# Performance work log

Hardware: AMD Instinct MI355X
Metric: run time of the kernel (lower is better)

## Reference

```python
import jax, jax.numpy as jnp
import numpy as np

N = 50000
E = 800000
IN_DIM, HID, LAT, DEC_HID = 256, 256, 128, 512


def _glorot(key, shape):
    fan_in, fan_out = shape
    lim = np.sqrt(6.0 / (fan_in + fan_out))
    return jax.random.uniform(key, shape, jnp.float32, -lim, lim)


def setup_inputs() -> dict:
    key = jax.random.key(0)
    ks = jax.random.split(key, 10)
    x = jax.random.normal(ks[0], (N, IN_DIM), jnp.float32)
    edge_index = jax.random.randint(ks[1], (2, E), 0, N, dtype=jnp.int64)
    return {
        "x": x,
        "edge_index": edge_index,
        "W1": _glorot(ks[2], (IN_DIM, HID)), "b1": jnp.zeros((HID,), jnp.float32),
        "W2": _glorot(ks[3], (HID, LAT)), "b2": jnp.zeros((LAT,), jnp.float32),
        "Wd1": _glorot(ks[4], (LAT, DEC_HID)), "bd1": jnp.zeros((DEC_HID,), jnp.float32),
        "Wd2": _glorot(ks[5], (DEC_HID, IN_DIM)), "bd2": jnp.zeros((IN_DIM,), jnp.float32),
    }


def _gcn_layer(x, src, dst, W, b, num_nodes):
    # linear transform
    xt = x @ W + b                      # [N, out]
    # scatter-mean aggregation over incoming edges (PyG aggr='mean')
    msg = xt[src]                       # [E, out] gather of source features
    summed = jax.ops.segment_sum(msg, dst, num_segments=num_nodes)
    cnt = jax.ops.segment_sum(jnp.ones((src.shape[0],), xt.dtype), dst,
                              num_segments=num_nodes)
    mean = summed / jnp.maximum(cnt, 1.0)[:, None]   # 0 for isolated nodes
    # relu + residual
    return jax.nn.relu(mean) + xt


def reference(x, edge_index, W1, b1, W2, b2, Wd1, bd1, Wd2, bd2):
    src, dst = edge_index[0], edge_index[1]
    h = _gcn_layer(x, src, dst, W1, b1, x.shape[0])
    z = _gcn_layer(h, src, dst, W2, b2, x.shape[0])
    # decoder MLP
    x_hat = jax.nn.relu(z @ Wd1 + bd1) @ Wd2 + bd2
    return (x_hat, z)
```

## Files before the change

### kernel.cpp

```cpp
#include <hip/hip_runtime.h>
#include <hip/hip_bf16.h>

#define TPB 256

typedef __attribute__((ext_vector_type(8))) short short8;
typedef __attribute__((ext_vector_type(4))) float f32x4;

__device__ __forceinline__ unsigned short f2bf(float f) {
    unsigned int u = __float_as_uint(f);
    u = (u + 0x7FFFu + ((u >> 16) & 1u)) >> 16;
    return (unsigned short)u;
}
__device__ __forceinline__ float bflo(unsigned int u) { return __uint_as_float(u << 16); }
__device__ __forceinline__ float bfhi(unsigned int u) { return __uint_as_float(u & 0xFFFF0000u); }

__device__ __forceinline__ void gload16(const void* g, void* l) {
    __builtin_amdgcn_global_load_lds(
        (const __attribute__((address_space(1))) unsigned int*)g,
        (__attribute__((address_space(3))) unsigned int*)l, 16, 0, 0);
}

__global__ void transpose_convert_all(
    const float* __restrict__ Wa, unsigned short* __restrict__ Ta, int Ka, int Na,
    const float* __restrict__ Wb, unsigned short* __restrict__ Tb, int Kb, int Nb,
    const float* __restrict__ Wc, unsigned short* __restrict__ Tc, int Kc, int Nc_,
    const float* __restrict__ Wd, unsigned short* __restrict__ Td, int Kd, int Nd)
{
    __shared__ float tile[32][33];
    int b = blockIdx.x;
    const float* W; unsigned short* T; int K, Nn;
    const int ta = (Na / 32) * (Ka / 32);
    const int tb = (Nb / 32) * (Kb / 32);
    const int tc = (Nc_ / 32) * (Kc / 32);
    if (b < ta)                { W = Wa; T = Ta; K = Ka; Nn = Na; }
    else if (b < ta + tb)      { b -= ta;           W = Wb; T = Tb; K = Kb; Nn = Nb; }
    else if (b < ta + tb + tc) { b -= ta + tb;      W = Wc; T = Tc; K = Kc; Nn = Nc_; }
    else                       { b -= ta + tb + tc; W = Wd; T = Td; K = Kd; Nn = Nd; }
    const int nx = Nn / 32;
    const int n0 = (b % nx) * 32;
    const int k0 = (b / nx) * 32;
    const int tx = threadIdx.x, ty = threadIdx.y;
#pragma unroll
    for (int i = 0; i < 4; ++i)
        tile[ty + i * 8][tx] = W[(size_t)(k0 + ty + i * 8) * Nn + n0 + tx];
    __syncthreads();
#pragma unroll
    for (int i = 0; i < 4; ++i)
        T[(size_t)(n0 + ty + i * 8) * K + k0 + tx] = f2bf(tile[tx][ty + i * 8]);
}

__device__ __forceinline__ void load_a16f(const float* p, short8& lo, short8& hi) {
    float4 f0 = *reinterpret_cast<const float4*>(p);
    float4 f1 = *reinterpret_cast<const float4*>(p + 4);
    float4 f2 = *reinterpret_cast<const float4*>(p + 8);
    float4 f3 = *reinterpret_cast<const float4*>(p + 12);
    lo[0] = (short)f2bf(f0.x); lo[1] = (short)f2bf(f0.y);
    lo[2] = (short)f2bf(f0.z); lo[3] = (short)f2bf(f0.w);
    lo[4] = (short)f2bf(f1.x); lo[5] = (short)f2bf(f1.y);
    lo[6] = (short)f2bf(f1.z); lo[7] = (short)f2bf(f1.w);
    hi[0] = (short)f2bf(f2.x); hi[1] = (short)f2bf(f2.y);
    hi[2] = (short)f2bf(f2.z); hi[3] = (short)f2bf(f2.w);
    hi[4] = (short)f2bf(f3.x); hi[5] = (short)f2bf(f3.y);
    hi[6] = (short)f2bf(f3.z); hi[7] = (short)f2bf(f3.w);
}

__device__ __forceinline__ void copy_out32(unsigned short* C, const float* Cst, const float* bias,
                                           int rowbase, int bn, int M, int Nc, int t, bool doRelu) {
#pragma unroll
    for (int it = 0; it < 2; ++it) {
        const int idx = it * 2048 + t * 8;
        const int row = idx >> 7, col = idx & 127;
        const int m = rowbase + row;
        if (m >= M) continue;
        float4 v0 = *reinterpret_cast<const float4*>(&Cst[idx]);
        float4 v1 = *reinterpret_cast<const float4*>(&Cst[idx + 4]);
        float4 b0 = *reinterpret_cast<const float4*>(&bias[bn + col]);
        float4 b1 = *reinterpret_cast<const float4*>(&bias[bn + col + 4]);
        float o[8] = {v0.x + b0.x, v0.y + b0.y, v0.z + b0.z, v0.w + b0.w,
                      v1.x + b1.x, v1.y + b1.y, v1.z + b1.z, v1.w + b1.w};
        short8 s;
#pragma unroll
        for (int j = 0; j < 8; ++j) {
            const float vv = doRelu ? fmaxf(o[j], 0.f) : o[j];
            s[j] = (short)f2bf(vv);
        }
        *reinterpret_cast<short8*>(&C[(size_t)m * Nc + bn + col]) = s;
    }
}
__device__ __forceinline__ void copy_out32(float* C, const float* Cst, const float* bias,
                                           int rowbase, int bn, int M, int Nc, int t, bool doRelu) {
#pragma unroll
    for (int it = 0; it < 4; ++it) {
        const int idx = it * 1024 + t * 4;
        const int row = idx >> 7, col = idx & 127;
        const int m = rowbase + row;
        if (m >= M) continue;
        float4 v = *reinterpret_cast<const float4*>(&Cst[idx]);
        float4 b = *reinterpret_cast<const float4*>(&bias[bn + col]);
        v.x += b.x; v.y += b.y; v.z += b.z; v.w += b.w;
        if (doRelu) {
            v.x = fmaxf(v.x, 0.f); v.y = fmaxf(v.y, 0.f);
            v.z = fmaxf(v.z, 0.f); v.w = fmaxf(v.w, 0.f);
        }
        *reinterpret_cast<float4*>(&C[(size_t)m * Nc + bn + col]) = v;
    }
}

template <typename TA, typename TC, int K, bool RELU>
__global__ __launch_bounds__(256) void mfma_gemm4(
    const TA* __restrict__ A, const unsigned short* __restrict__ Bt,
    const float* __restrict__ bias, TC* __restrict__ C, int M, int Nc)
{
    __shared__ unsigned short lds_s[2][12288];
    constexpr bool AF32 = (sizeof(TA) == 4);

    const int t  = threadIdx.x;
    const int l  = t & 63;
    const int w  = t >> 6;
    const int wm = w >> 1, wn = w & 1;
    const int bm = blockIdx.x * 64;
    const int bn = blockIdx.y * 128;

    f32x4 acc[2][4] = {};

    const int r4 = t >> 2;
    const int q4 = t & 3;
    const int gmr = bm + r4;
    short8 sa0, sa1;

    auto loadAregs = [&](int k0) {
        if (gmr < M) load_a16f((const float*)A + (size_t)gmr * K + k0 + q4 * 16, sa0, sa1);
        else { sa0 = (short8)0; sa1 = (short8)0; }
    };
    auto writeAregs = [&](int buf) {
        const int s0 = (2 * q4)     ^ (r4 & 7);
        const int s1 = (2 * q4 + 1) ^ (r4 & 7);
        *reinterpret_cast<short8*>(&lds_s[buf][r4 * 64 + s0 * 8]) = sa0;
        *reinterpret_cast<short8*>(&lds_s[buf][r4 * 64 + s1 * 8]) = sa1;
    };
    auto stageA_lds = [&](int buf, int k0) {
#pragma unroll
        for (int ii = 0; ii < 2; ++ii) {
            const int seg = w + ii * 4;
            const int rr  = seg * 8 + (l >> 3);
            const int ss  = l & 7;
            const int gr  = min(bm + rr, M - 1);
            gload16((const unsigned short*)A + (size_t)gr * K + k0 + ((ss ^ (rr & 7)) * 8),
                    &lds_s[buf][seg * 512]);
        }
    };
    auto stageB = [&](int buf, int k0) {
#pragma unroll
        for (int ii = 0; ii < 4; ++ii) {
            const int seg = w + ii * 4;
            const int rr  = seg * 8 + (l >> 3);
            const int ss  = l & 7;
            gload16(Bt + (size_t)(bn + rr) * K + k0 + ((ss ^ (rr & 7)) * 8),
                    &lds_s[buf][4096 + seg * 512]);
        }
    };

    constexpr int S = K / 64;

    if (AF32) {
        loadAregs(0);
        writeAregs(0);
        if (S > 1) loadAregs(64);
    } else {
        stageA_lds(0, 0);
    }
    stageB(0, 0);
    __syncthreads();

#pragma unroll
    for (int step = 0; step < S; ++step) {
        const int k0  = step * 64;
        const int cur = step & 1;

        if (step + 1 < S) {
            if (AF32) writeAregs(cur ^ 1);
            else      stageA_lds(cur ^ 1, k0 + 64);
            stageB(cur ^ 1, k0 + 64);
        }
        if (AF32 && step + 2 < S) loadAregs(k0 + 128);

#pragma unroll
        for (int kk = 0; kk < 2; ++kk) {
            short8 af[2], bf4[4];
#pragma unroll
            for (int mf = 0; mf < 2; ++mf) {
                const int row  = wm * 32 + mf * 16 + (l & 15);
                const int slot = (kk * 4 + (l >> 4)) ^ (row & 7);
                af[mf] = *reinterpret_cast<const short8*>(&lds_s[cur][row * 64 + slot * 8]);
            }
#pragma unroll
            for (int nf = 0; nf < 4; ++nf) {
                const int row  = wn * 64 + nf * 16 + (l & 15);
                const int slot = (kk * 4 + (l >> 4)) ^ (row & 7);
                bf4[nf] = *reinterpret_cast<const short8*>(&lds_s[cur][4096 + row * 64 + slot * 8]);
            }
#pragma unroll
            for (int mf = 0; mf < 2; ++mf)
#pragma unroll
                for (int nf = 0; nf < 4; ++nf)
                    acc[mf][nf] = __builtin_amdgcn_mfma_f32_16x16x32_bf16(
                        af[mf], bf4[nf], acc[mf][nf], 0, 0, 0);
        }
        __syncthreads();
    }

    float* Cst = reinterpret_cast<float*>(lds_s);
#pragma unroll
    for (int p = 0; p < 2; ++p) {
        if (wm == p) {
#pragma unroll
            for (int mf = 0; mf < 2; ++mf)
#pragma unroll
                for (int nf = 0; nf < 4; ++nf)
#pragma unroll
                    for (int rr = 0; rr < 4; ++rr) {
                        const int row = mf * 16 + (l >> 4) * 4 + rr;
                        const int col = wn * 64 + nf * 16 + (l & 15);
                        Cst[row * 128 + col] = acc[mf][nf][rr];
                    }
        }
        __syncthreads();
        copy_out32(C, Cst, bias, bm + p * 32, bn, M, Nc, t, RELU);
        if (p == 0) __syncthreads();
    }
}

__global__ void hist_kernel(const int* __restrict__ dst, int* __restrict__ counts,
                            int E, int csz)
{
    const int chunk = blockIdx.x & 7;
    const int blk   = blockIdx.x >> 3;
    const int lo = chunk * csz, hi = lo + csz;
    const int base = (blk * TPB + threadIdx.x) * 4;
    if (base + 3 < E) {
        int4 d4 = *reinterpret_cast<const int4*>(dst + base);
        if (d4.x >= lo && d4.x < hi) atomicAdd(&counts[d4.x], 1);
        if (d4.y >= lo && d4.y < hi) atomicAdd(&counts[d4.y], 1);
        if (d4.z >= lo && d4.z < hi) atomicAdd(&counts[d4.z], 1);
        if (d4.w >= lo && d4.w < hi) atomicAdd(&counts[d4.w], 1);
    } else {
        for (int e = base; e < E; ++e) {
            const int d = dst[e];
            if (d >= lo && d < hi) atomicAdd(&counts[d], 1);
        }
    }
}

__global__ void scan1_kernel(const int* __restrict__ counts,
                             int* __restrict__ local, int* __restrict__ bsum, int N)
{
    __shared__ int sh[TPB];
    const int t = threadIdx.x;
    const int base = blockIdx.x * 1024 + t * 4;
    int v[4];
#pragma unroll
    for (int i = 0; i < 4; ++i) v[i] = (base + i < N) ? counts[base + i] : 0;
    const int s = v[0] + v[1] + v[2] + v[3];
    sh[t] = s;
    __syncthreads();
    for (int d = 1; d < TPB; d <<= 1) {
        int x = (t >= d) ? sh[t - d] : 0;
        __syncthreads();
        sh[t] += x;
        __syncthreads();
    }
    int run = sh[t] - s;
#pragma unroll
    for (int i = 0; i < 4; ++i) {
        if (base + i < N) local[base + i] = run;
        run += v[i];
    }
    if (t == TPB - 1) bsum[blockIdx.x] = sh[TPB - 1];
}

__global__ void scan2_kernel(int* __restrict__ bsum, int nb)
{
    __shared__ int sh[TPB];
    const int t = threadIdx.x;
    const int v = (t < nb) ? bsum[t] : 0;
    sh[t] = v;
    __syncthreads();
    for (int d = 1; d < TPB; d <<= 1) {
        int x = (t >= d) ? sh[t - d] : 0;
        __syncthreads();
        sh[t] += x;
        __syncthreads();
    }
    if (t < nb) bsum[t] = sh[t] - v;
}

__global__ void scan3_kernel(int* __restrict__ offsets, int* __restrict__ cursor,
                             const int* __restrict__ bsum, int N)
{
    const int i = blockIdx.x * TPB + threadIdx.x;
    if (i < N) {
        const int o = offsets[i] + bsum[i >> 10];
        offsets[i] = o;
        cursor[i]  = o;
    }
}

__global__ void build_perm_kernel(const int* __restrict__ src, const int* __restrict__ dst,
                                  int* __restrict__ cursor, int* __restrict__ perm,
                                  int E, int csz)
{
    const int chunk = blockIdx.x & 7;
    const int blk   = blockIdx.x >> 3;
    const int lo = chunk * csz, hi = lo + csz;
    const int base = (blk * TPB + threadIdx.x) * 4;
    if (base + 3 < E) {
        int4 d4 = *reinterpret_cast<const int4*>(dst + base);
        if (d4.x >= lo && d4.x < hi) { int p = atomicAdd(&cursor[d4.x], 1); perm[p] = src[base + 0]; }
        if (d4.y >= lo && d4.y < hi) { int p = atomicAdd(&cursor[d4.y], 1); perm[p] = src[base + 1]; }
        if (d4.z >= lo && d4.z < hi) { int p = atomicAdd(&cursor[d4.z], 1); perm[p] = src[base + 2]; }
        if (d4.w >= lo && d4.w < hi) { int p = atomicAdd(&cursor[d4.w], 1); perm[p] = src[base + 3]; }
    } else {
        for (int e = base; e < E; ++e) {
            const int d = dst[e];
            if (d >= lo && d < hi) { int p = atomicAdd(&cursor[d], 1); perm[p] = src[e]; }
        }
    }
}

template <int F, int CH, bool WRITE_ZF32>
__global__ __launch_bounds__(256) void agg_kernel(
    const uint2* __restrict__ xt,
    const int* __restrict__ offsets, const int* __restrict__ counts,
    const int* __restrict__ perm,
    uint2* __restrict__ out, float* __restrict__ zf32, int N)
{
    constexpr int RU  = F / 4;
    constexpr int L   = RU / CH;
    constexpr int NPB = TPB / L;

    const int chunk = blockIdx.x % CH;
    const int node  = (blockIdx.x / CH) * NPB + threadIdx.x / L;
    const int g     = threadIdx.x % L;
    if (node >= N) return;
    const int col = chunk * L + g;

    const int start = offsets[node];
    const int deg   = counts[node];

    float a0 = 0.f, a1 = 0.f, a2 = 0.f, a3 = 0.f;

    for (int base = 0; base < deg; base += L) {
        const int m = min(L, deg - base);
        const int pidx = perm[start + base + ((g < m) ? g : (m - 1))];
        int j = 0;
        for (; j + 4 <= m; j += 4) {
            const int s0 = __shfl(pidx, j + 0, L);
            const int s1 = __shfl(pidx, j + 1, L);
            const int s2 = __shfl(pidx, j + 2, L);
            const int s3 = __shfl(pidx, j + 3, L);
            const uint2 v0 = xt[(size_t)s0 * RU + col];
            const uint2 v1 = xt[(size_t)s1 * RU + col];
            const uint2 v2 = xt[(size_t)s2 * RU + col];
            const uint2 v3 = xt[(size_t)s3 * RU + col];
            a0 += bflo(v0.x) + bflo(v1.x) + bflo(v2.x) + bflo(v3.x);
            a1 += bfhi(v0.x) + bfhi(v1.x) + bfhi(v2.x) + bfhi(v3.x);
            a2 += bflo(v0.y) + bflo(v1.y) + bflo(v2.y) + bflo(v3.y);
            a3 += bfhi(v0.y) + bfhi(v1.y) + bfhi(v2.y) + bfhi(v3.y);
        }
        for (; j < m; ++j) {
            const int s = __shfl(pidx, j, L);
            const uint2 v = xt[(size_t)s * RU + col];
            a0 += bflo(v.x); a1 += bfhi(v.x);
            a2 += bflo(v.y); a3 += bfhi(v.y);
        }
    }

    const float c = (float)max(deg, 1);
    const uint2 xv = xt[(size_t)node * RU + col];
    const float r0 = fmaxf(a0 / c, 0.f) + bflo(xv.x);
    const float r1 = fmaxf(a1 / c, 0.f) + bfhi(xv.x);
    const float r2 = fmaxf(a2 / c, 0.f) + bflo(xv.y);
    const float r3 = fmaxf(a3 / c, 0.f) + bfhi(xv.y);

    uint2 o;
    o.x = (unsigned int)f2bf(r0) | ((unsigned int)f2bf(r1) << 16);
    o.y = (unsigned int)f2bf(r2) | ((unsigned int)f2bf(r3) << 16);
    out[(size_t)node * RU + col] = o;
    if (WRITE_ZF32) {
        float4 z4 = make_float4(r0, r1, r2, r3);
        *reinterpret_cast<float4*>(&zf32[(size_t)node * F + 4 * col]) = z4;
    }
}

extern "C" void kernel_launch(void* const* d_in, const int* in_sizes, int n_in,
                              void* d_out, int out_size, void* d_ws, size_t ws_size,
                              hipStream_t stream)
{
    const int IN_DIM = 256, HID = 256, LAT = 128, DEC_HID = 512;
    const int N = in_sizes[0] / IN_DIM;
    const int E = in_sizes[1] / 2;

    const float* x   = (const float*)d_in[0];
    const int*   ei  = (const int*)d_in[1];
    const float* W1  = (const float*)d_in[2];
    const float* b1  = (const float*)d_in[3];
    const float* W2  = (const float*)d_in[4];
    const float* b2  = (const float*)d_in[5];
    const float* Wd1 = (const float*)d_in[6];
    const float* bd1 = (const float*)d_in[7];
    const float* Wd2 = (const float*)d_in[8];
    const float* bd2 = (const float*)d_in[9];

    const int* src = ei;
    const int* dst = ei + E;

    unsigned short* xt1  = (unsigned short*)d_ws;
    unsigned short* h    = xt1  + (size_t)N * 256;
    unsigned short* xt2  = h    + (size_t)N * 256;
    unsigned short* zbf  = xt2  + (size_t)N * 128;
    unsigned short* hdec = zbf  + (size_t)N * 128;
    unsigned short* wt1  = hdec + (size_t)N * 512;
    unsigned short* wt2  = wt1  + 256 * 256;
    unsigned short* wtd1 = wt2  + 128 * 256;
    unsigned short* wtd2 = wtd1 + 512 * 128;
    int* counts  = (int*)(wtd2 + 256 * 512);
    int* offsets = counts + N;
    int* cursor  = offsets + N;
    int* bsum    = cursor + N;
    int* perm    = bsum + 256;

    float* out_xhat = (float*)d_out;
    float* out_z    = out_xhat + (size_t)N * IN_DIM;

    dim3 blk(TPB);
    const int mb64 = (N + 63) / 64;
    const int nscan = (N + 1023) / 1024;
    const int csz = (N + 7) / 8;
    const int egrid8 = ((E + TPB * 4 - 1) / (TPB * 4)) * 8;

    {
        const int tiles = (HID/32)*(IN_DIM/32) + (LAT/32)*(HID/32)
                        + (DEC_HID/32)*(LAT/32) + (IN_DIM/32)*(DEC_HID/32);
        transpose_convert_all<<<tiles, dim3(32, 8), 0, stream>>>(
            W1, wt1, IN_DIM, HID,  W2, wt2, HID, LAT,
            Wd1, wtd1, LAT, DEC_HID,  Wd2, wtd2, DEC_HID, IN_DIM);
    }

    hipMemsetAsync(counts, 0, (size_t)N * 4, stream);
    hist_kernel<<<egrid8, blk, 0, stream>>>(dst, counts, E, csz);
    scan1_kernel<<<nscan, blk, 0, stream>>>(counts, offsets, bsum, N);
    scan2_kernel<<<1, blk, 0, stream>>>(bsum, nscan);
    scan3_kernel<<<(N + TPB - 1) / TPB, blk, 0, stream>>>(offsets, cursor, bsum, N);
    build_perm_kernel<<<egrid8, blk, 0, stream>>>(src, dst, cursor, perm, E, csz);

    mfma_gemm4<float, unsigned short, 256, false><<<dim3(mb64, HID / 128), blk, 0, stream>>>(
        x, wt1, b1, xt1, N, HID);
    {
        const int ngroups = (N + 15) / 16;
        agg_kernel<256, 4, false><<<ngroups * 4, blk, 0, stream>>>(
            (const uint2*)xt1, offsets, counts, perm, (uint2*)h, nullptr, N);
    }

    mfma_gemm4<unsigned short, unsigned short, 256, false><<<dim3(mb64, LAT / 128), blk, 0, stream>>>(
        h, wt2, b2, xt2, N, LAT);
    {
        const int ngroups = (N + 15) / 16;
        agg_kernel<128, 2, true><<<ngroups * 2, blk, 0, stream>>>(
            (const uint2*)xt2, offsets, counts, perm, (uint2*)zbf, out_z, N);
    }

    mfma_gemm4<unsigned short, unsigned short, 128, true><<<dim3(mb64, DEC_HID / 128), blk, 0, stream>>>(
        zbf, wtd1, bd1, hdec, N, DEC_HID);
    mfma_gemm4<unsigned short, float, 512, false><<<dim3(mb64, IN_DIM / 128), blk, 0, stream>>>(
        hdec, wtd2, bd2, out_xhat, N, IN_DIM);
}
```

Measured before the change: 272.0 us.

## Fuse decoder MLP into one kernel keeping hidden activations in LDS

Replaces the two decoder GEMM launches with one fused kernel. Each block takes 32 rows of z and computes the 512-wide ReLU hidden layer into LDS as bf16, then multiplies it by Wd2 to write x_hat. This removes the global write and read of the N×512 hidden tensor and one launch. In exchange, blocks use about 72KB of LDS, which limits occupancy. Weight tiles are also reloaded for every 32-row block, and loads are not double-buffered.

```diff
diff --git a/kernel.cpp b/kernel.cpp
--- a/kernel.cpp
+++ b/kernel.cpp
@@ -227,6 +227,154 @@
         __syncthreads();
         copy_out32(C, Cst, bias, bm + p * 32, bn, M, Nc, t, RELU);
         if (p == 0) __syncthreads();
+    }
+}
+
+__global__ __launch_bounds__(256) void fused_decoder(
+    const unsigned short* __restrict__ Z,
+    const unsigned short* __restrict__ Wt1,
+    const float* __restrict__ b1v,
+    const unsigned short* __restrict__ Wt2,
+    const float* __restrict__ b2v,
+    float* __restrict__ Xh, int M)
+{
+    __shared__ unsigned short z_s[4096];
+    __shared__ unsigned short hd_s[16384];
+    __shared__ unsigned short b_s[16384];
+
+    const int t = threadIdx.x;
+    const int l = t & 63;
+    const int w = t >> 6;
+    const int bm = blockIdx.x * 32;
+
+#pragma unroll
+    for (int ii = 0; ii < 2; ++ii) {
+        const int seg = w + ii * 4;
+        const int r   = seg * 4 + (l >> 4);
+        const int sl  = l & 15;
+        const int gr  = min(bm + r, M - 1);
+        gload16(Z + (size_t)gr * 128 + ((sl ^ (r & 15)) * 8), &z_s[seg * 512]);
+    }
+
+    auto stageB = [&](const unsigned short* W, int Krow, int rowbase, int k0) {
+#pragma unroll
+        for (int ii = 0; ii < 8; ++ii) {
+            const int seg = w + ii * 4;
+            const int rr  = seg * 8 + (l >> 3);
+            const int sl  = l & 7;
+            gload16(W + (size_t)(rowbase + rr) * Krow + k0 + ((sl ^ (rr & 7)) * 8),
+                    &b_s[seg * 512]);
+        }
+    };
+
+    f32x4 acc[2][4];
+
+#pragma unroll
+    for (int p = 0; p < 4; ++p) {
+        const int nc = p >> 1, st = p & 1;
+        stageB(Wt1, 128, nc * 256, st * 64);
+        __syncthreads();
+        if (st == 0) {
+#pragma unroll
+            for (int mf = 0; mf < 2; ++mf)
+#pragma unroll
+                for (int nf = 0; nf < 4; ++nf) acc[mf][nf] = (f32x4)(0.f);
+        }
+#pragma unroll
+        for (int kk = 0; kk < 2; ++kk) {
+            const int kc  = st * 8 + kk * 4 + (l >> 4);
+            const int kc2 = kk * 4 + (l >> 4);
+            short8 af[2], bf[4];
+#pragma unroll
+            for (int mf = 0; mf < 2; ++mf) {
+                const int r = mf * 16 + (l & 15);
+                af[mf] = *reinterpret_cast<const short8*>(&z_s[r * 128 + ((kc ^ (r & 15)) * 8)]);
+            }
+#pragma unroll
+            for (int nf = 0; nf < 4; ++nf) {
+                const int r = w * 64 + nf * 16 + (l & 15);
+                bf[nf] = *reinterpret_cast<const short8*>(&b_s[r * 64 + ((kc2 ^ (r & 7)) * 8)]);
+            }
+#pragma unroll
+            for (int mf = 0; mf < 2; ++mf)
+#pragma unroll
+                for (int nf = 0; nf < 4; ++nf)
+                    acc[mf][nf] = __builtin_amdgcn_mfma_f32_16x16x32_bf16(
+                        af[mf], bf[nf], acc[mf][nf], 0, 0, 0);
+        }
+        if (st == 1) {
+#pragma unroll
+            for (int mf = 0; mf < 2; ++mf)
+#pragma unroll
+                for (int nf = 0; nf < 4; ++nf) {
+                    const int c  = nc * 256 + w * 64 + nf * 16 + (l & 15);
+                    const float bv = b1v[c];
+#pragma unroll
+                    for (int rr = 0; rr < 4; ++rr) {
+                        const int r = mf * 16 + (l >> 4) * 4 + rr;
+                        const float v = fmaxf(acc[mf][nf][rr] + bv, 0.f);
+                        hd_s[r * 512 + (((c >> 3) ^ (r & 7)) * 8) + (c & 7)] = f2bf(v);
+                    }
+                }
+        }
+        __syncthreads();
+    }
+
+#pragma unroll
+    for (int mf = 0; mf < 2; ++mf)
+#pragma unroll
+        for (int nf = 0; nf < 4; ++nf) acc[mf][nf] = (f32x4)(0.f);
+
+    for (int step = 0; step < 8; ++step) {
+        stageB(Wt2, 512, 0, step * 64);
+        __syncthreads();
+#pragma unroll
+        for (int kk = 0; kk < 2; ++kk) {
+            const int kc  = step * 8 + kk * 4 + (l >> 4);
+            const int kc2 = kk * 4 + (l >> 4);
+            short8 af[2], bf[4];
+#pragma unroll
+            for (int mf = 0; mf < 2; ++mf) {
+                const int r = mf * 16 + (l & 15);
+                af[mf] = *reinterpret_cast<const short8*>(&hd_s[r * 512 + ((kc ^ (r & 7)) * 8)]);
+            }
+#pragma unroll
+            for (int nf = 0; nf < 4; ++nf) {
+                const int r = w * 64 + nf * 16 + (l & 15);
+                bf[nf] = *reinterpret_cast<const short8*>(&b_s[r * 64 + ((kc2 ^ (r & 7)) * 8)]);
+            }
+#pragma unroll
+            for (int mf = 0; mf < 2; ++mf)
+#pragma unroll
+                for (int nf = 0; nf < 4; ++nf)
+                    acc[mf][nf] = __builtin_amdgcn_mfma_f32_16x16x32_bf16(
+                        af[mf], bf[nf], acc[mf][nf], 0, 0, 0);
+        }
+        __syncthreads();
+    }
+
+    float* Cst = reinterpret_cast<float*>(b_s);
+#pragma unroll
+    for (int mf = 0; mf < 2; ++mf)
+#pragma unroll
+        for (int nf = 0; nf < 4; ++nf)
+#pragma unroll
+            for (int rr = 0; rr < 4; ++rr) {
+                const int r = mf * 16 + (l >> 4) * 4 + rr;
+                const int c = w * 64 + nf * 16 + (l & 15);
+                Cst[r * 256 + c] = acc[mf][nf][rr];
+            }
+    __syncthreads();
+#pragma unroll
+    for (int it = 0; it < 8; ++it) {
+        const int idx = it * 1024 + t * 4;
+        const int r = idx >> 8, c = idx & 255;
+        if (bm + r < M) {
+            float4 v = *reinterpret_cast<const float4*>(&Cst[idx]);
+            float4 b = *reinterpret_cast<const float4*>(&b2v[c]);
+            v.x += b.x; v.y += b.y; v.z += b.z; v.w += b.w;
+            *reinterpret_cast<float4*>(&Xh[(size_t)(bm + r) * 256 + c]) = v;
+        }
     }
 }
 
@@ -469,8 +617,6 @@
             (const uint2*)xt2, offsets, counts, perm, (uint2*)zbf, out_z, N);
     }
 
-    mfma_gemm4<unsigned short, unsigned short, 128, true><<<dim3(mb64, DEC_HID / 128), blk, 0, stream>>>(
-        zbf, wtd1, bd1, hdec, N, DEC_HID);
-    mfma_gemm4<unsigned short, float, 512, false><<<dim3(mb64, IN_DIM / 128), blk, 0, stream>>>(
-        hdec, wtd2, bd2, out_xhat, N, IN_DIM);
-}
+    fused_decoder<<<(N + 31) / 32, blk, 0, stream>>>(
+        zbf, wtd1, bd1, wtd2, bd2, out_xhat, N);
+}
```

New measurement: 267.0 us. Within noise of the previous version (-1.8%).
